# Kernel optimization log

Hardware: AMD Instinct MI355X
Metric: run time of the kernel (lower is better)

Reference implementation:

```python
import jax, jax.numpy as jnp
import numpy as np

EPS = 1e-05


def setup_inputs() -> dict:
    key = jax.random.key(0)
    k1, k2, k3 = jax.random.split(key, 3)
    b, s, n, m = 16, 4096, 1024, 1024
    x = jax.random.normal(k1, (b, s, n), dtype=jnp.float32)
    # torch.rand -> uniform [0,1)
    A = jax.random.uniform(k2, (m, n), dtype=jnp.float32)
    B = jax.random.uniform(k3, (m, n), dtype=jnp.float32)
    return {"x": x, "A": A, "B": B}


def reference(x, A, B):
    # query: project each token with A, then sum over seq -> [b, m]
    query = jnp.einsum('ij,bsj->bi', A, x)  # fused projection + seq-sum
    query = query / (EPS + jnp.linalg.norm(query, axis=1, keepdims=True))
    # keys: [b, s, m], L2-normalized per token
    keys = jnp.einsum('ij,bsj->bsi', B, x)
    keys = keys / (EPS + jnp.linalg.norm(keys, axis=2, keepdims=True))
    # cosine-style similarity (no softmax): [b, s]
    sim = jnp.einsum('bi,bsi->bs', query, keys)
    # weighted sum of raw inputs: [b, n]
    out = jnp.einsum('bs,bsn->bn', sim, x)
    return (out, sim)
```

## Files before the change

### kernel.cpp

```cpp
#include <hip/hip_runtime.h>

#define EPS 1e-5f

typedef __bf16 bf16x8 __attribute__((ext_vector_type(8)));
typedef __bf16 bf16x4 __attribute__((ext_vector_type(4)));
typedef float f32x4 __attribute__((ext_vector_type(4)));

static __device__ __forceinline__ unsigned int f2bf(float f) {
    unsigned int u = __builtin_bit_cast(unsigned int, f);
    u = (u + 0x7fffu + ((u >> 16) & 1u)) >> 16;
    return u;
}
static __device__ __forceinline__ float bf2f(unsigned int lo16) {
    unsigned int u = lo16 << 16;
    return __builtin_bit_cast(float, u);
}

static __device__ __forceinline__ void gll16(const void* g, void* l) {
    __builtin_amdgcn_global_load_lds(
        (const __attribute__((address_space(1))) unsigned int*)(unsigned long long)g,
        (__attribute__((address_space(3))) unsigned int*)(unsigned int)(unsigned long long)l,
        16, 0, 0);
}

template <int XBF>
__global__ __launch_bounds__(256) void k_prep(const float* __restrict__ x,
                                              float* __restrict__ xs_part,
                                              unsigned short* __restrict__ xbf) {
    const int b = blockIdx.y, sc = blockIdx.x, tid = threadIdx.x;
    const size_t rowbase = ((size_t)(b * 4096 + sc * 128)) * 1024;
    const float4* src = (const float4*)(x + rowbase) + tid;
    uint2* dst = XBF ? ((uint2*)(xbf + rowbase) + tid) : (uint2*)0;
    float ax = 0.f, ay = 0.f, az = 0.f, aw = 0.f;
    for (int r = 0; r < 128; ++r) {
        float4 v = src[r * 256];
        ax += v.x; ay += v.y; az += v.z; aw += v.w;
        if (XBF) {
            uint2 p;
            p.x = f2bf(v.x) | (f2bf(v.y) << 16);
            p.y = f2bf(v.z) | (f2bf(v.w) << 16);
            dst[r * 256] = p;
        }
    }
    float4 o; o.x = ax; o.y = ay; o.z = az; o.w = aw;
    ((float4*)(xs_part + ((size_t)(b * 32 + sc)) * 1024))[tid] = o;
}

__global__ __launch_bounds__(256) void k_glue(const float* __restrict__ B,
                                              unsigned short* __restrict__ Bb,
                                              const float* __restrict__ xs_part,
                                              const float* __restrict__ A,
                                              float* __restrict__ q) {
    __shared__ float xsl[1024];
    const int blk = blockIdx.x, tid = threadIdx.x;
    if (blk < 1024) {
        const int i = blk * 256 + tid;
        float4 v = ((const float4*)B)[i];
        uint2 p;
        p.x = f2bf(v.x) | (f2bf(v.y) << 16);
        p.y = f2bf(v.z) | (f2bf(v.w) << 16);
        ((uint2*)Bb)[i] = p;
        return;
    }
    const int gb = blk - 1024;
    const int g = gb & 3, b = gb >> 2;
    {
        float4 s4 = {0.f, 0.f, 0.f, 0.f};
        const float4* p = (const float4*)(xs_part + (size_t)b * 32768) + tid;
        for (int sc = 0; sc < 32; ++sc) {
            float4 v = p[sc * 256];
            s4.x += v.x; s4.y += v.y; s4.z += v.z; s4.w += v.w;
        }
        ((float4*)xsl)[tid] = s4;
    }
    __syncthreads();
    const int i = g * 256 + tid;
    const float4* ar = (const float4*)(A + (size_t)i * 1024);
    float acc = 0.f;
    for (int k = 0; k < 256; ++k) {
        float4 a = ar[k], v = ((const float4*)xsl)[k];
        acc += a.x * v.x + a.y * v.y + a.z * v.z + a.w * v.w;
    }
    q[b * 1024 + i] = acc;
}

__global__ __launch_bounds__(256) void k_wf(const float* __restrict__ B,
                                            const float* __restrict__ q,
                                            float* __restrict__ w) {
    __shared__ float ql[1024];
    __shared__ float wsum[4];
    const int b = blockIdx.y, g = blockIdx.x, tid = threadIdx.x;
    float4 v = ((const float4*)(q + (size_t)b * 1024))[tid];
    float ss = v.x * v.x + v.y * v.y + v.z * v.z + v.w * v.w;
    for (int o = 1; o < 64; o <<= 1) ss += __shfl_xor(ss, o);
    if ((tid & 63) == 0) wsum[tid >> 6] = ss;
    __syncthreads();
    const float inv = 1.f / (EPS + sqrtf(wsum[0] + wsum[1] + wsum[2] + wsum[3]));
    float4 n; n.x = v.x * inv; n.y = v.y * inv; n.z = v.z * inv; n.w = v.w * inv;
    ((float4*)ql)[tid] = n;
    __syncthreads();
    const int j = g * 256 + tid;
    float acc = 0.f;
    for (int i = 0; i < 1024; ++i) acc += B[(size_t)i * 1024 + j] * ql[i];
    w[b * 1024 + j] = acc;
}

#define FENCE asm volatile("" ::: "memory")

__global__ __launch_bounds__(512, 2) void k_main2(const unsigned short* __restrict__ xbf,
                                                  const unsigned short* __restrict__ Bb,
                                                  const float* __restrict__ w,
                                                  float* __restrict__ out,
                                                  float* __restrict__ sim_out) {
    __shared__ __align__(16) unsigned short Xs[2][256 * 64];
    __shared__ __align__(16) unsigned short Bs[2][256 * 64];
    __shared__ float nsq_s[256];
    __shared__ float numer_s[256];
    __shared__ float simv_s[256];
    __shared__ float wlds[1024];

    const int tid = threadIdx.x;
    const int lane = tid & 63;
    const int l15 = lane & 15, lg = lane >> 4;
    const int w8 = tid >> 6;
    const int wm = w8 >> 2, wn = w8 & 3;
    const int bx = blockIdx.x;
    const size_t tok0 = (size_t)bx * 256;
    const int b = bx >> 4;

    ((float2*)wlds)[tid] = ((const float2*)(w + (size_t)b * 1024))[tid];
    if (tid < 256) nsq_s[tid] = 0.f;
    __syncthreads();

#define STAGE(s_, buf_)                                                                  \
    do {                                                                                 \
        const int mt_ = (s_) >> 4, ks_ = (s_) & 15;                                      \
        _Pragma("unroll") for (int it = 0; it < 4; ++it) {                               \
            const int g_ = it * 512 + tid;                                               \
            const int row_ = g_ >> 3, c_ = g_ & 7;                                       \
            const int csw_ = (c_ ^ (row_ & 7)) * 8;                                      \
            gll16(xbf + (tok0 + row_) * 1024 + ks_ * 64 + csw_,                          \
                  (char*)Xs[buf_] + (size_t)(it * 512 + (tid & ~63)) * 16);              \
            gll16(Bb + (size_t)(mt_ * 256 + row_) * 1024 + ks_ * 64 + csw_,              \
                  (char*)Bs[buf_] + (size_t)(it * 512 + (tid & ~63)) * 16);              \
        }                                                                                \
    } while (0)

    f32x4 acc[8][4];
    float numer_acc = 0.f;
    const int ntok = tid >> 1, nhalf = tid & 1;
    const int nswt = (ntok & 7) << 4;

    STAGE(0, 0);
    STAGE(1, 1);

    for (int s = 0; s < 64; ++s) {
        const int buf = s & 1;
        if ((s & 15) == 0) {
#pragma unroll
            for (int mi = 0; mi < 8; ++mi)
#pragma unroll
                for (int ni = 0; ni < 4; ++ni) acc[mi][ni] = (f32x4){0.f, 0.f, 0.f, 0.f};
        }
        if (s < 62) asm volatile("s_waitcnt vmcnt(8)" ::: "memory");
        else        asm volatile("s_waitcnt vmcnt(0)" ::: "memory");
        __builtin_amdgcn_s_barrier();

        const char* xb = (const char*)Xs[buf] + (wm * 128 + l15) * 128;
        const char* bb = (const char*)Bs[buf] + (wn * 64 + l15) * 128;
        const int sw = (l15 & 7) << 4;

        bf16x8 bq[4][2];
#pragma unroll
        for (int ni = 0; ni < 4; ++ni)
#pragma unroll
            for (int kk = 0; kk < 2; ++kk)
                bq[ni][kk] = *(const bf16x8*)(bb + ni * 16 * 128 + ((kk * 64 + lg * 16) ^ sw));

        __builtin_amdgcn_s_setprio(1);
#pragma unroll
        for (int p = 0; p < 4; ++p) {
            bf16x8 a[2][2];
#pragma unroll
            for (int mi = 0; mi < 2; ++mi)
#pragma unroll
                for (int kk = 0; kk < 2; ++kk)
                    a[mi][kk] = *(const bf16x8*)(xb + (p * 2 + mi) * 16 * 128 +
                                                 ((kk * 64 + lg * 16) ^ sw));
#pragma unroll
            for (int mi = 0; mi < 2; ++mi)
#pragma unroll
                for (int ni = 0; ni < 4; ++ni)
#pragma unroll
                    for (int kk = 0; kk < 2; ++kk)
                        acc[p * 2 + mi][ni] = __builtin_amdgcn_mfma_f32_16x16x32_bf16(
                            a[mi][kk], bq[ni][kk], acc[p * 2 + mi][ni], 0, 0, 0);
        }
        __builtin_amdgcn_s_setprio(0);

        if (s < 16) {
            const char* pt = (const char*)Xs[buf] + ntok * 128;
            const float* wp = wlds + s * 64 + nhalf * 32;
            float na = 0.f;
#pragma unroll
            for (int j = 0; j < 4; ++j) {
                bf16x8 v = *(const bf16x8*)(pt + ((nhalf * 64 + j * 16) ^ nswt));
#pragma unroll
                for (int e = 0; e < 8; ++e) na += (float)v[e] * wp[j * 8 + e];
            }
            numer_acc += na;
        }

        FENCE;
        __builtin_amdgcn_s_barrier();
        FENCE;
        if (s + 2 < 64) STAGE(s + 2, buf);

        if ((s & 15) == 15) {
#pragma unroll
            for (int mi = 0; mi < 8; ++mi)
#pragma unroll
                for (int r = 0; r < 4; ++r) {
                    float v = 0.f;
#pragma unroll
                    for (int ni = 0; ni < 4; ++ni) v += acc[mi][ni][r] * acc[mi][ni][r];
                    v += __shfl_xor(v, 1);
                    v += __shfl_xor(v, 2);
                    v += __shfl_xor(v, 4);
                    v += __shfl_xor(v, 8);
                    if (l15 == 0) atomicAdd(&nsq_s[wm * 128 + mi * 16 + lg * 4 + r], v);
                }
        }
        if (s == 15) {
            float na = numer_acc + __shfl_xor(numer_acc, 1);
            if (nhalf == 0) numer_s[ntok] = na;
        }
    }
#undef STAGE

    __syncthreads();
    if (tid < 256) {
        float sv = numer_s[tid] / (EPS + sqrtf(nsq_s[tid]));
        simv_s[tid] = sv;
        sim_out[tok0 + tid] = sv;
    }
    __syncthreads();

    {
        const unsigned short* xp = xbf + tok0 * 1024 + tid * 2;
        float oa0 = 0.f, oa1 = 0.f;
#pragma unroll 8
        for (int t = 0; t < 256; ++t) {
            unsigned int u = *(const unsigned int*)(xp + (size_t)t * 1024);
            float sv = simv_s[t];
            oa0 += sv * bf2f(u & 0xffffu);
            oa1 += sv * bf2f(u >> 16);
        }
        float* dst = out + (size_t)b * 1024 + tid * 2;
        atomicAdd(dst + 0, oa0);
        atomicAdd(dst + 1, oa1);
    }
}

__global__ __launch_bounds__(256, 2) void k_nsq_f32(const float* __restrict__ x,
                                                    const unsigned short* __restrict__ Bb,
                                                    float* __restrict__ nsq_g) {
    __shared__ unsigned short Xs[128 * 64];
    __shared__ unsigned short Bs[128 * 64];
    __shared__ float nsq_s[128];

    const int tid = threadIdx.x;
    const int lane = tid & 63;
    const int l15 = lane & 15, lg = lane >> 4;
    const int w = tid >> 6;
    const int wr = w >> 1, wc = w & 1;
    const int st = blockIdx.x * 128;
    const int mh = blockIdx.y;

    float nsq_reg[4][4];
#pragma unroll
    for (int mi = 0; mi < 4; ++mi)
#pragma unroll
        for (int r = 0; r < 4; ++r) nsq_reg[mi][r] = 0.f;

    for (int mti = 0; mti < 4; ++mti) {
        const int mt = mh * 4 + mti;
        f32x4 acc[4][4];
#pragma unroll
        for (int mi = 0; mi < 4; ++mi)
#pragma unroll
            for (int ni = 0; ni < 4; ++ni) acc[mi][ni] = (f32x4){0.f, 0.f, 0.f, 0.f};

        for (int ks = 0; ks < 16; ++ks) {
            __syncthreads();
            {
                const int row = tid >> 1, kh = tid & 1;
                const float* srcx = x + (size_t)(st + row) * 1024 + ks * 64 + kh * 32;
                char* ldsrow = (char*)Xs + row * 128;
                const int sw = (row & 7) << 4;
#pragma unroll
                for (int j = 0; j < 4; ++j) {
                    float4 v0 = ((const float4*)srcx)[j * 2];
                    float4 v1 = ((const float4*)srcx)[j * 2 + 1];
                    uint4 p;
                    p.x = f2bf(v0.x) | (f2bf(v0.y) << 16);
                    p.y = f2bf(v0.z) | (f2bf(v0.w) << 16);
                    p.z = f2bf(v1.x) | (f2bf(v1.y) << 16);
                    p.w = f2bf(v1.z) | (f2bf(v1.w) << 16);
                    *(uint4*)(ldsrow + (((kh * 4 + j) * 16) ^ sw)) = p;
                }
#pragma unroll
                for (int it = 0; it < 4; ++it) {
                    const int idx = it * 256 + tid;
                    const int brow = idx >> 3, c = idx & 7;
                    char* baseB = (char*)Bs + (size_t)(it * 256 + (tid & ~63)) * 16;
                    gll16(Bb + (size_t)(mt * 128 + brow) * 1024 + ks * 64 + (c ^ (brow & 7)) * 8,
                          baseB);
                }
            }
            __syncthreads();

            const char* xb = (const char*)Xs + (wr * 64 + l15) * 128;
            const char* bb = (const char*)Bs + (wc * 64 + l15) * 128;
            const int sw = (l15 & 7) << 4;
#pragma unroll
            for (int kk = 0; kk < 2; ++kk) {
                const int ob = (kk * 64 + lg * 16) ^ sw;
                bf16x8 a[4], bq[4];
#pragma unroll
                for (int mi = 0; mi < 4; ++mi) a[mi] = *(const bf16x8*)(xb + mi * 2048 + ob);
#pragma unroll
                for (int ni = 0; ni < 4; ++ni) bq[ni] = *(const bf16x8*)(bb + ni * 2048 + ob);
#pragma unroll
                for (int mi = 0; mi < 4; ++mi)
#pragma unroll
                    for (int ni = 0; ni < 4; ++ni)
                        acc[mi][ni] = __builtin_amdgcn_mfma_f32_16x16x32_bf16(
                            a[mi], bq[ni], acc[mi][ni], 0, 0, 0);
            }
        }
#pragma unroll
        for (int mi = 0; mi < 4; ++mi)
#pragma unroll
            for (int ni = 0; ni < 4; ++ni)
#pragma unroll
                for (int r = 0; r < 4; ++r)
                    nsq_reg[mi][r] += acc[mi][ni][r] * acc[mi][ni][r];
    }

    if (tid < 128) nsq_s[tid] = 0.f;
    __syncthreads();
#pragma unroll
    for (int mi = 0; mi < 4; ++mi)
#pragma unroll
        for (int r = 0; r < 4; ++r) {
            float v = nsq_reg[mi][r];
            v += __shfl_xor(v, 1);
            v += __shfl_xor(v, 2);
            v += __shfl_xor(v, 4);
            v += __shfl_xor(v, 8);
            if (l15 == 0) atomicAdd(&nsq_s[wr * 64 + mi * 16 + lg * 4 + r], v);
        }
    __syncthreads();
    if (tid < 128) nsq_g[(size_t)mh * 65536 + st + tid] = nsq_s[tid];
}

__global__ __launch_bounds__(256, 2) void k_finish0(
    const float* __restrict__ x, const float* __restrict__ w,
    const float* __restrict__ nsq_g, float* __restrict__ outp,
    float* __restrict__ sim_out) {
    __shared__ __align__(16) unsigned short xt[32 * 1024];
    __shared__ float numer[32];
    __shared__ float simv[32];

    const int tid = threadIdx.x;
    const int bs = blockIdx.x;
    const int b = bs >> 7, s0 = (bs & 127) * 32;
    const size_t tok0 = (size_t)b * 4096 + s0;

    const float4* src = (const float4*)(x + tok0 * 1024) + tid;
    char* lds = (char*)xt;
    for (int r = 0; r < 32; ++r) {
        float4 v = src[r * 256];
        uint2 p;
        p.x = f2bf(v.x) | (f2bf(v.y) << 16);
        p.y = f2bf(v.z) | (f2bf(v.w) << 16);
        *(uint2*)(lds + r * 2048 + ((tid * 8) ^ ((r & 7) << 4))) = p;
    }
    __syncthreads();

    {
        const int t = tid >> 3, kp = tid & 7;
        const float* wb = w + (size_t)b * 1024 + kp * 128;
        const char* pt = (const char*)xt + t * 2048;
        const int sw2 = (t & 7) << 4;
        float acc = 0.f;
#pragma unroll
        for (int j = 0; j < 16; ++j) {
            const int kb = (kp * 128 + j * 8) * 2;
            bf16x8 v = *(const bf16x8*)(pt + (kb ^ sw2));
#pragma unroll
            for (int e = 0; e < 8; ++e) acc += (float)v[e] * wb[j * 8 + e];
        }
        acc += __shfl_xor(acc, 1);
        acc += __shfl_xor(acc, 2);
        acc += __shfl_xor(acc, 4);
        if (kp == 0) numer[t] = acc;
    }
    __syncthreads();

    if (tid < 32) {
        float nt = nsq_g[tok0 + tid] + nsq_g[65536 + tok0 + tid];
        float s = numer[tid] / (EPS + sqrtf(nt));
        simv[tid] = s;
        sim_out[tok0 + tid] = s;
    }
    __syncthreads();

    {
        const int n0 = tid * 4;
        float a0 = 0.f, a1 = 0.f, a2 = 0.f, a3 = 0.f;
        const char* p = (const char*)xt;
#pragma unroll 4
        for (int t = 0; t < 32; ++t) {
            int byte = t * 2048 + ((n0 * 2) ^ ((t & 7) << 4));
            bf16x4 v = *(const bf16x4*)(p + byte);
            float s = simv[t];
            a0 += s * (float)v[0];
            a1 += s * (float)v[1];
            a2 += s * (float)v[2];
            a3 += s * (float)v[3];
        }
        float4 o; o.x = a0; o.y = a1; o.z = a2; o.w = a3;
        ((float4*)(outp + (size_t)bs * 1024))[tid] = o;
    }
}

template <int NT>
__global__ void k_outred(const float* __restrict__ outp, float* __restrict__ out) {
    const int b = blockIdx.y, j = blockIdx.x * 256 + threadIdx.x;
    const float* p = outp + (size_t)b * NT * 1024 + j;
    float s = 0.f;
    for (int t = 0; t < NT; ++t) s += p[t * 1024];
    out[b * 1024 + j] = s;
}

extern "C" void kernel_launch(void* const* d_in, const int* in_sizes, int n_in,
                              void* d_out, int out_size, void* d_ws, size_t ws_size,
                              hipStream_t stream) {
    const float* x = (const float*)d_in[0];
    const float* A = (const float*)d_in[1];
    const float* B = (const float*)d_in[2];
    float* out = (float*)d_out;
    float* sim = out + 16 * 1024;
    float* ws = (float*)d_ws;
    float* xs_part = ws;
    float* q = ws + 540672;
    float* wv = ws + 557056;
    float* nsq = ws + 573440;
    float* outp = ws + 704512;
    unsigned short* Bb = (unsigned short*)(ws + 2801664);
    unsigned short* xbf = (unsigned short*)(ws + 3325952);
    const bool xb = ws_size >= (size_t)(3325952 + 33554432) * 4;

    if (xb) {
        hipMemsetAsync(d_out, 0, 16 * 1024 * sizeof(float), stream);
        k_prep<1><<<dim3(32, 16), 256, 0, stream>>>(x, xs_part, xbf);
        k_glue<<<1088, 256, 0, stream>>>(B, Bb, xs_part, A, q);
        k_wf<<<dim3(4, 16), 256, 0, stream>>>(B, q, wv);
        k_main2<<<256, 512, 0, stream>>>(xbf, Bb, wv, out, sim);
    } else {
        k_prep<0><<<dim3(32, 16), 256, 0, stream>>>(x, xs_part, (unsigned short*)0);
        k_glue<<<1088, 256, 0, stream>>>(B, Bb, xs_part, A, q);
        k_wf<<<dim3(4, 16), 256, 0, stream>>>(B, q, wv);
        k_nsq_f32<<<dim3(512, 2), 256, 0, stream>>>(x, Bb, nsq);
        k_finish0<<<2048, 256, 0, stream>>>(x, wv, nsq, outp, sim);
        k_outred<128><<<dim3(4, 16), 256, 0, stream>>>(outp, out);
    }
}
```

Before: 305.6 us.

## Shrink main fused GEMM tile to 128x128 with 256 threads and vectorize k_wf

```diff
diff --git a/kernel.cpp b/kernel.cpp
--- a/kernel.cpp
+++ b/kernel.cpp
@@ -89,7 +89,7 @@
                                             float* __restrict__ w) {
     __shared__ float ql[1024];
     __shared__ float wsum[4];
-    const int b = blockIdx.y, g = blockIdx.x, tid = threadIdx.x;
+    const int b = blockIdx.x, tid = threadIdx.x;
     float4 v = ((const float4*)(q + (size_t)b * 1024))[tid];
     float ss = v.x * v.x + v.y * v.y + v.z * v.z + v.w * v.w;
     for (int o = 1; o < 64; o <<= 1) ss += __shfl_xor(ss, o);
@@ -99,54 +99,58 @@
     float4 n; n.x = v.x * inv; n.y = v.y * inv; n.z = v.z * inv; n.w = v.w * inv;
     ((float4*)ql)[tid] = n;
     __syncthreads();
-    const int j = g * 256 + tid;
-    float acc = 0.f;
-    for (int i = 0; i < 1024; ++i) acc += B[(size_t)i * 1024 + j] * ql[i];
-    w[b * 1024 + j] = acc;
+    float4 acc = {0.f, 0.f, 0.f, 0.f};
+    const float4* Br = (const float4*)B + tid;
+    for (int i = 0; i < 1024; ++i) {
+        float4 br = Br[(size_t)i * 256];
+        float qi = ql[i];
+        acc.x += br.x * qi; acc.y += br.y * qi; acc.z += br.z * qi; acc.w += br.w * qi;
+    }
+    ((float4*)(w + (size_t)b * 1024))[tid] = acc;
 }
 
 #define FENCE asm volatile("" ::: "memory")
 
-__global__ __launch_bounds__(512, 2) void k_main2(const unsigned short* __restrict__ xbf,
+__global__ __launch_bounds__(256, 2) void k_main3(const unsigned short* __restrict__ xbf,
                                                   const unsigned short* __restrict__ Bb,
                                                   const float* __restrict__ w,
                                                   float* __restrict__ out,
                                                   float* __restrict__ sim_out) {
-    __shared__ __align__(16) unsigned short Xs[2][256 * 64];
-    __shared__ __align__(16) unsigned short Bs[2][256 * 64];
-    __shared__ float nsq_s[256];
-    __shared__ float numer_s[256];
-    __shared__ float simv_s[256];
+    __shared__ __align__(16) unsigned short Xs[2][128 * 64];
+    __shared__ __align__(16) unsigned short Bs[2][128 * 64];
+    __shared__ float nsq_s[128];
+    __shared__ float numer_s[128];
+    __shared__ float simv_s[128];
     __shared__ float wlds[1024];
 
     const int tid = threadIdx.x;
     const int lane = tid & 63;
     const int l15 = lane & 15, lg = lane >> 4;
-    const int w8 = tid >> 6;
-    const int wm = w8 >> 2, wn = w8 & 3;
+    const int w4 = tid >> 6;
+    const int wm = w4 >> 1, wn = w4 & 1;
     const int bx = blockIdx.x;
-    const size_t tok0 = (size_t)bx * 256;
-    const int b = bx >> 4;
-
-    ((float2*)wlds)[tid] = ((const float2*)(w + (size_t)b * 1024))[tid];
-    if (tid < 256) nsq_s[tid] = 0.f;
+    const size_t tok0 = (size_t)bx * 128;
+    const int b = bx >> 5;
+
+    ((float4*)wlds)[tid] = ((const float4*)(w + (size_t)b * 1024))[tid];
+    if (tid < 128) nsq_s[tid] = 0.f;
     __syncthreads();
 
 #define STAGE(s_, buf_)                                                                  \
     do {                                                                                 \
         const int mt_ = (s_) >> 4, ks_ = (s_) & 15;                                      \
         _Pragma("unroll") for (int it = 0; it < 4; ++it) {                               \
-            const int g_ = it * 512 + tid;                                               \
+            const int g_ = it * 256 + tid;                                               \
             const int row_ = g_ >> 3, c_ = g_ & 7;                                       \
             const int csw_ = (c_ ^ (row_ & 7)) * 8;                                      \
             gll16(xbf + (tok0 + row_) * 1024 + ks_ * 64 + csw_,                          \
-                  (char*)Xs[buf_] + (size_t)(it * 512 + (tid & ~63)) * 16);              \
-            gll16(Bb + (size_t)(mt_ * 256 + row_) * 1024 + ks_ * 64 + csw_,              \
-                  (char*)Bs[buf_] + (size_t)(it * 512 + (tid & ~63)) * 16);              \
+                  (char*)Xs[buf_] + (size_t)(it * 256 + (tid & ~63)) * 16);              \
+            gll16(Bb + (size_t)(mt_ * 128 + row_) * 1024 + ks_ * 64 + csw_,              \
+                  (char*)Bs[buf_] + (size_t)(it * 256 + (tid & ~63)) * 16);              \
         }                                                                                \
     } while (0)
 
-    f32x4 acc[8][4];
+    f32x4 acc[4][4];
     float numer_acc = 0.f;
     const int ntok = tid >> 1, nhalf = tid & 1;
     const int nswt = (ntok & 7) << 4;
@@ -154,48 +158,41 @@
     STAGE(0, 0);
     STAGE(1, 1);
 
-    for (int s = 0; s < 64; ++s) {
+    for (int s = 0; s < 128; ++s) {
         const int buf = s & 1;
         if ((s & 15) == 0) {
 #pragma unroll
-            for (int mi = 0; mi < 8; ++mi)
+            for (int mi = 0; mi < 4; ++mi)
 #pragma unroll
                 for (int ni = 0; ni < 4; ++ni) acc[mi][ni] = (f32x4){0.f, 0.f, 0.f, 0.f};
         }
-        if (s < 62) asm volatile("s_waitcnt vmcnt(8)" ::: "memory");
-        else        asm volatile("s_waitcnt vmcnt(0)" ::: "memory");
+        if (s < 126) asm volatile("s_waitcnt vmcnt(8)" ::: "memory");
+        else         asm volatile("s_waitcnt vmcnt(0)" ::: "memory");
         __builtin_amdgcn_s_barrier();
 
-        const char* xb = (const char*)Xs[buf] + (wm * 128 + l15) * 128;
+        const char* xb = (const char*)Xs[buf] + (wm * 64 + l15) * 128;
         const char* bb = (const char*)Bs[buf] + (wn * 64 + l15) * 128;
         const int sw = (l15 & 7) << 4;
 
-        bf16x8 bq[4][2];
-#pragma unroll
-        for (int ni = 0; ni < 4; ++ni)
-#pragma unroll
-            for (int kk = 0; kk < 2; ++kk)
-                bq[ni][kk] = *(const bf16x8*)(bb + ni * 16 * 128 + ((kk * 64 + lg * 16) ^ sw));
+        bf16x8 a[4][2], bq[4][2];
+#pragma unroll
+        for (int kk = 0; kk < 2; ++kk) {
+            const int ob = (kk * 64 + lg * 16) ^ sw;
+#pragma unroll
+            for (int mi = 0; mi < 4; ++mi) a[mi][kk] = *(const bf16x8*)(xb + mi * 16 * 128 + ob);
+#pragma unroll
+            for (int ni = 0; ni < 4; ++ni) bq[ni][kk] = *(const bf16x8*)(bb + ni * 16 * 128 + ob);
+        }
 
         __builtin_amdgcn_s_setprio(1);
 #pragma unroll
-        for (int p = 0; p < 4; ++p) {
-            bf16x8 a[2][2];
-#pragma unroll
-            for (int mi = 0; mi < 2; ++mi)
-#pragma unroll
-                for (int kk = 0; kk < 2; ++kk)
-                    a[mi][kk] = *(const bf16x8*)(xb + (p * 2 + mi) * 16 * 128 +
-                                                 ((kk * 64 + lg * 16) ^ sw));
-#pragma unroll
-            for (int mi = 0; mi < 2; ++mi)
+        for (int kk = 0; kk < 2; ++kk)
+#pragma unroll
+            for (int mi = 0; mi < 4; ++mi)
 #pragma unroll
                 for (int ni = 0; ni < 4; ++ni)
-#pragma unroll
-                    for (int kk = 0; kk < 2; ++kk)
-                        acc[p * 2 + mi][ni] = __builtin_amdgcn_mfma_f32_16x16x32_bf16(
-                            a[mi][kk], bq[ni][kk], acc[p * 2 + mi][ni], 0, 0, 0);
-        }
+                    acc[mi][ni] = __builtin_amdgcn_mfma_f32_16x16x32_bf16(
+                        a[mi][kk], bq[ni][kk], acc[mi][ni], 0, 0, 0);
         __builtin_amdgcn_s_setprio(0);
 
         if (s < 16) {
@@ -214,11 +211,11 @@
         FENCE;
         __builtin_amdgcn_s_barrier();
         FENCE;
-        if (s + 2 < 64) STAGE(s + 2, buf);
+        if (s + 2 < 128) STAGE(s + 2, buf);
 
         if ((s & 15) == 15) {
 #pragma unroll
-            for (int mi = 0; mi < 8; ++mi)
+            for (int mi = 0; mi < 4; ++mi)
 #pragma unroll
                 for (int r = 0; r < 4; ++r) {
                     float v = 0.f;
@@ -228,7 +225,7 @@
                     v += __shfl_xor(v, 2);
                     v += __shfl_xor(v, 4);
                     v += __shfl_xor(v, 8);
-                    if (l15 == 0) atomicAdd(&nsq_s[wm * 128 + mi * 16 + lg * 4 + r], v);
+                    if (l15 == 0) atomicAdd(&nsq_s[wm * 64 + mi * 16 + lg * 4 + r], v);
                 }
         }
         if (s == 15) {
@@ -239,7 +236,7 @@
 #undef STAGE
 
     __syncthreads();
-    if (tid < 256) {
+    if (tid < 128) {
         float sv = numer_s[tid] / (EPS + sqrtf(nsq_s[tid]));
         simv_s[tid] = sv;
         sim_out[tok0 + tid] = sv;
@@ -247,18 +244,22 @@
     __syncthreads();
 
     {
-        const unsigned short* xp = xbf + tok0 * 1024 + tid * 2;
-        float oa0 = 0.f, oa1 = 0.f;
+        const unsigned short* xp = xbf + tok0 * 1024 + tid * 4;
+        float oa0 = 0.f, oa1 = 0.f, oa2 = 0.f, oa3 = 0.f;
 #pragma unroll 8
-        for (int t = 0; t < 256; ++t) {
-            unsigned int u = *(const unsigned int*)(xp + (size_t)t * 1024);
+        for (int t = 0; t < 128; ++t) {
+            uint2 u = *(const uint2*)(xp + (size_t)t * 1024);
             float sv = simv_s[t];
-            oa0 += sv * bf2f(u & 0xffffu);
-            oa1 += sv * bf2f(u >> 16);
-        }
-        float* dst = out + (size_t)b * 1024 + tid * 2;
+            oa0 += sv * bf2f(u.x & 0xffffu);
+            oa1 += sv * bf2f(u.x >> 16);
+            oa2 += sv * bf2f(u.y & 0xffffu);
+            oa3 += sv * bf2f(u.y >> 16);
+        }
+        float* dst = out + (size_t)b * 1024 + tid * 4;
         atomicAdd(dst + 0, oa0);
         atomicAdd(dst + 1, oa1);
+        atomicAdd(dst + 2, oa2);
+        atomicAdd(dst + 3, oa3);
     }
 }
 
@@ -467,12 +468,12 @@
         hipMemsetAsync(d_out, 0, 16 * 1024 * sizeof(float), stream);
         k_prep<1><<<dim3(32, 16), 256, 0, stream>>>(x, xs_part, xbf);
         k_glue<<<1088, 256, 0, stream>>>(B, Bb, xs_part, A, q);
-        k_wf<<<dim3(4, 16), 256, 0, stream>>>(B, q, wv);
-        k_main2<<<256, 512, 0, stream>>>(xbf, Bb, wv, out, sim);
+        k_wf<<<16, 256, 0, stream>>>(B, q, wv);
+        k_main3<<<512, 256, 0, stream>>>(xbf, Bb, wv, out, sim);
     } else {
         k_prep<0><<<dim3(32, 16), 256, 0, stream>>>(x, xs_part, (unsigned short*)0);
         k_glue<<<1088, 256, 0, stream>>>(B, Bb, xs_part, A, q);
-        k_wf<<<dim3(4, 16), 256, 0, stream>>>(B, q, wv);
+        k_wf<<<16, 256, 0, stream>>>(B, q, wv);
         k_nsq_f32<<<dim3(512, 2), 256, 0, stream>>>(x, Bb, nsq);
         k_finish0<<<2048, 256, 0, stream>>>(x, wv, nsq, outp, sim);
         k_outred<128><<<dim3(4, 16), 256, 0, stream>>>(outp, out);
```

Result: slower. 344.4 us (+12.7%).
